# Kernel optimization log

Hardware: AMD Instinct MI355X
Metric: run time of the kernel (lower is better)

## Reference

```python
import jax, jax.numpy as jnp
import numpy as np

D_MODEL = 1024
NHEAD = 16
HEAD_DIM = D_MODEL // NHEAD


def setup_inputs() -> dict:
    key = jax.random.key(0)
    ks = jax.random.split(key, 9)
    B, N = 2, 2048
    x = jax.random.normal(ks[0], (B, N, D_MODEL), dtype=jnp.float32)
    s = 1.0 / np.sqrt(D_MODEL)
    Wq = jax.random.normal(ks[1], (D_MODEL, D_MODEL), dtype=jnp.float32) * s
    bq = jnp.zeros((D_MODEL,), dtype=jnp.float32)
    Wk = jax.random.normal(ks[2], (D_MODEL, D_MODEL), dtype=jnp.float32) * s
    bk = jnp.zeros((D_MODEL,), dtype=jnp.float32)
    Wv = jax.random.normal(ks[3], (D_MODEL, D_MODEL), dtype=jnp.float32) * s
    bv = jnp.zeros((D_MODEL,), dtype=jnp.float32)
    Wo = jax.random.normal(ks[4], (D_MODEL, D_MODEL), dtype=jnp.float32) * s
    bo = jnp.zeros((D_MODEL,), dtype=jnp.float32)
    return {"x": x, "Wq": Wq, "bq": bq, "Wk": Wk, "bk": bk,
            "Wv": Wv, "bv": bv, "Wo": Wo, "bo": bo}


def reference(x, Wq, bq, Wk, bk, Wv, bv, Wo, bo):
    B, N, C = x.shape
    H, Dh = NHEAD, HEAD_DIM
    scale = 1.0 / np.sqrt(Dh)

    def split_heads(t):
        # [B, N, C] -> [B, H, N, Dh]
        return t.reshape(B, N, H, Dh).transpose(0, 2, 1, 3)

    q = split_heads(x @ Wq.T + bq)
    k = split_heads(x @ Wk.T + bk)
    v = split_heads(x @ Wv.T + bv)

    # bipolar transform on Q/K before scores
    qb = (q - 0.5) * 2.0
    kb = (k - 0.5) * 2.0

    scores = jnp.einsum('bhqd,bhkd->bhqk', qb, kb) * scale  # [B,H,N,N]
    attn = jax.nn.softmax(scores, axis=-1)
    out = jnp.einsum('bhqk,bhkd->bhqd', attn, v)  # [B,H,N,Dh]
    out = out.transpose(0, 2, 1, 3).reshape(B, N, C)
    return out @ Wo.T + bo
```

## Files before the change

kernel.cpp:

```cpp
#include <hip/hip_runtime.h>
#include <cstdint>
#include <math.h>

typedef __attribute__((ext_vector_type(8))) short short8;
typedef __attribute__((ext_vector_type(4))) short shortx4;
typedef __attribute__((ext_vector_type(4))) float floatx4;
typedef __attribute__((ext_vector_type(16))) float floatx16;

#define D_MODEL 1024
#define NHEAD   16
#define HDIM    64
#define BATCH   2
#define SEQ     2048
#define MTOT    (BATCH*SEQ)

#if __has_builtin(__builtin_amdgcn_exp2f)
#define EXP2(x) __builtin_amdgcn_exp2f(x)
#else
#define EXP2(x) exp2f(x)
#endif

__device__ __forceinline__ short f2bf(float f) {
    union { float f; uint32_t u; } v; v.f = f;
    uint32_t u = v.u;
    uint32_t r = (u + 0x7fffu + ((u >> 16) & 1u)) >> 16;
    return (short)(uint16_t)r;
}

__device__ __forceinline__ unsigned pk2(float lo, float hi) {
    union { float f; uint32_t u; } x, y; x.f = lo; y.f = hi;
    return __builtin_amdgcn_perm(y.u + 0x8000u, x.u + 0x8000u, 0x07060302u);
}

__device__ __forceinline__ void async16(const short* g, short* l) {
    __builtin_amdgcn_global_load_lds((__attribute__((address_space(1))) void*)g,
                                     (__attribute__((address_space(3))) void*)l,
                                     16, 0, 0);
}

__global__ __launch_bounds__(256) void cast_all_kernel(
    const float* __restrict__ x,  const float* __restrict__ Wq, const float* __restrict__ Wk,
    const float* __restrict__ Wv, const float* __restrict__ Wo,
    short* __restrict__ xb, short* __restrict__ wqb, short* __restrict__ wkb,
    short* __restrict__ wvb, short* __restrict__ wob)
{
    const int i = blockIdx.x * 256 + threadIdx.x;
    const float* src; short* dst; int off;
    if (i < 524288) { src = x; dst = xb; off = i; }
    else {
        const int j = i - 524288;
        const int seg = j >> 17, o = j & 131071;
        src = (seg == 0) ? Wq : (seg == 1) ? Wk : (seg == 2) ? Wv : Wo;
        dst = (seg == 0) ? wqb : (seg == 1) ? wkb : (seg == 2) ? wvb : wob;
        off = o;
    }
    const floatx4* p = (const floatx4*)(src + (size_t)off * 8);
    floatx4 a = p[0], b = p[1];
    short8 r;
    r[0]=f2bf(a[0]); r[1]=f2bf(a[1]); r[2]=f2bf(a[2]); r[3]=f2bf(a[3]);
    r[4]=f2bf(b[0]); r[5]=f2bf(b[1]); r[6]=f2bf(b[2]); r[7]=f2bf(b[3]);
    *(short8*)(dst + (size_t)off * 8) = r;
}

__global__ __launch_bounds__(256, 3) void qkv_gemm_kernel(
    const short* __restrict__ Xb,
    const short* __restrict__ Wqb, const short* __restrict__ Wkb, const short* __restrict__ Wvb,
    const float* __restrict__ bq, const float* __restrict__ bk, const float* __restrict__ bv,
    short* __restrict__ Qo, short* __restrict__ Ko, short* __restrict__ Vo)
{
    const int mode = blockIdx.z;
    const short* W    = (mode == 0) ? Wqb : (mode == 1) ? Wkb : Wvb;
    const float* bias = (mode == 0) ? bq  : (mode == 1) ? bk  : bv;

    const int m_t = blockIdx.y * 128;
    const int n_t = blockIdx.x * 128;
    const int tid = threadIdx.x;
    const int lane = tid & 63, laneM = lane & 15, quad = lane >> 4;
    const int wave = tid >> 6;
    const int wm = (wave >> 1) * 64, wn = (wave & 1) * 64;

    __shared__ short la[2][128][4][8];
    __shared__ short lb[2][128][4][8];

    floatx4 acc[4][4];
#pragma unroll
    for (int mb = 0; mb < 4; mb++)
#pragma unroll
        for (int nb = 0; nb < 4; nb++) acc[mb][nb] = (floatx4){0.f,0.f,0.f,0.f};

#define QSTAGE(bf, kk)                                                                  \
    {                                                                                   \
        int c = tid;                                                                    \
        async16(Xb + (size_t)(m_t + (c >> 2)) * D_MODEL + (kk) + ((((c & 3) ^ ((c >> 3) & 3))) * 8), \
                &la[bf][0][0][0] + c * 8);                                              \
        c = tid + 256;                                                                  \
        async16(Xb + (size_t)(m_t + (c >> 2)) * D_MODEL + (kk) + ((((c & 3) ^ ((c >> 3) & 3))) * 8), \
                &la[bf][0][0][0] + c * 8);                                              \
        c = tid;                                                                        \
        async16(W  + (size_t)(n_t + (c >> 2)) * D_MODEL + (kk) + ((((c & 3) ^ ((c >> 3) & 3))) * 8), \
                &lb[bf][0][0][0] + c * 8);                                              \
        c = tid + 256;                                                                  \
        async16(W  + (size_t)(n_t + (c >> 2)) * D_MODEL + (kk) + ((((c & 3) ^ ((c >> 3) & 3))) * 8), \
                &lb[bf][0][0][0] + c * 8);                                              \
    }

    QSTAGE(0, 0)

    const int swz = (laneM >> 1) & 3;
    for (int it = 0; it < 32; ++it) {
        const int bf = it & 1;
        __syncthreads();

        short8 af[4], bfv[4];
#pragma unroll
        for (int mb = 0; mb < 4; mb++) af[mb]  = *(const short8*)&la[bf][wm + mb*16 + laneM][quad ^ swz][0];
#pragma unroll
        for (int nb = 0; nb < 4; nb++) bfv[nb] = *(const short8*)&lb[bf][wn + nb*16 + laneM][quad ^ swz][0];

        if (it < 31) QSTAGE(bf ^ 1, (it + 1) * 32)

#pragma unroll
        for (int mb = 0; mb < 4; mb++)
#pragma unroll
            for (int nb = 0; nb < 4; nb++)
                acc[mb][nb] = __builtin_amdgcn_mfma_f32_16x16x32_bf16(af[mb], bfv[nb], acc[mb][nb], 0, 0, 0);
    }
#undef QSTAGE

    if (mode == 2) {
#pragma unroll
        for (int nb = 0; nb < 4; nb++) {
            const int col = n_t + wn + nb*16 + laneM;
            const float bb = bias[col];
            const int h = col >> 6, d = col & 63;
#pragma unroll
            for (int mb = 0; mb < 4; mb++) {
                const int row0 = m_t + wm + mb*16 + quad*4;
                const int bi = row0 >> 11, seq0 = row0 & 2047;
                shortx4 sv;
#pragma unroll
                for (int r = 0; r < 4; r++) sv[r] = f2bf(acc[mb][nb][r] + bb);
                *(shortx4*)(Vo + ((size_t)(bi*NHEAD + h) * HDIM + d) * SEQ + seq0) = sv;
            }
        }
    } else {
        short* out = (mode == 0) ? Qo : Ko;
#pragma unroll
        for (int nb = 0; nb < 4; nb++) {
            const int col = n_t + wn + nb*16 + laneM;
            const float bb = bias[col];
            const int h = col >> 6, d = col & 63;
#pragma unroll
            for (int mb = 0; mb < 4; mb++) {
                const int row0 = m_t + wm + mb*16 + quad*4;
#pragma unroll
                for (int r = 0; r < 4; r++) {
                    float v = acc[mb][nb][r] + bb;
                    v = (mode == 0) ? (2.0f*v - 1.0f) * 0.18033688011112042f
                                    : (2.0f*v - 1.0f);
                    const int m = row0 + r;
                    const int bi = m >> 11, seq = m & 2047;
                    out[((size_t)(bi*NHEAD + h) * SEQ + seq) * HDIM + d] = f2bf(v);
                }
            }
        }
    }
}

__global__ __launch_bounds__(256, 3) void out_gemm_kernel(
    const short* __restrict__ Ab, const short* __restrict__ Wb,
    const float* __restrict__ bias, float* __restrict__ out)
{
    const int m_t = blockIdx.y * 128;
    const int n_t = blockIdx.x * 64;
    const int tid = threadIdx.x;
    const int lane = tid & 63, laneM = lane & 15, quad = lane >> 4;
    const int wave = tid >> 6;
    const int wm = (wave >> 1) * 64, wn = (wave & 1) * 32;

    __shared__ short la[2][128][4][8];
    __shared__ short lb[2][64][4][8];

    floatx4 acc[4][2];
#pragma unroll
    for (int mb = 0; mb < 4; mb++)
#pragma unroll
        for (int nb = 0; nb < 2; nb++) acc[mb][nb] = (floatx4){0.f,0.f,0.f,0.f};

#define OSTAGE(bf, kk)                                                                  \
    {                                                                                   \
        int c = tid;                                                                    \
        async16(Ab + (size_t)(m_t + (c >> 2)) * D_MODEL + (kk) + ((((c & 3) ^ ((c >> 3) & 3))) * 8), \
                &la[bf][0][0][0] + c * 8);                                              \
        c = tid + 256;                                                                  \
        async16(Ab + (size_t)(m_t + (c >> 2)) * D_MODEL + (kk) + ((((c & 3) ^ ((c >> 3) & 3))) * 8), \
                &la[bf][0][0][0] + c * 8);                                              \
        c = tid;                                                                        \
        async16(Wb + (size_t)(n_t + (c >> 2)) * D_MODEL + (kk) + ((((c & 3) ^ ((c >> 3) & 3))) * 8), \
                &lb[bf][0][0][0] + c * 8);                                              \
    }

    OSTAGE(0, 0)

    const int swz = (laneM >> 1) & 3;
    for (int it = 0; it < 32; ++it) {
        const int bf = it & 1;
        __syncthreads();

        short8 af[4], bfv[2];
#pragma unroll
        for (int mb = 0; mb < 4; mb++) af[mb]  = *(const short8*)&la[bf][wm + mb*16 + laneM][quad ^ swz][0];
#pragma unroll
        for (int nb = 0; nb < 2; nb++) bfv[nb] = *(const short8*)&lb[bf][wn + nb*16 + laneM][quad ^ swz][0];

        if (it < 31) OSTAGE(bf ^ 1, (it + 1) * 32)

#pragma unroll
        for (int mb = 0; mb < 4; mb++)
#pragma unroll
            for (int nb = 0; nb < 2; nb++)
                acc[mb][nb] = __builtin_amdgcn_mfma_f32_16x16x32_bf16(af[mb], bfv[nb], acc[mb][nb], 0, 0, 0);
    }
#undef OSTAGE

#pragma unroll
    for (int nb = 0; nb < 2; nb++) {
        const int col = n_t + wn + nb*16 + laneM;
        const float bb = bias[col];
#pragma unroll
        for (int mb = 0; mb < 4; mb++) {
            const int row0 = m_t + wm + mb*16 + quad*4;
#pragma unroll
            for (int r = 0; r < 4; r++)
                out[(size_t)(row0 + r) * D_MODEL + col] = acc[mb][nb][r] + bb;
        }
    }
}

__global__ __launch_bounds__(512, 4) void attn_kernel(const short* __restrict__ Qb,
                                                      const short* __restrict__ Kb,
                                                      const short* __restrict__ Vt,
                                                      short* __restrict__ Ob)
{
    const int bh = blockIdx.y;
    const int q0 = blockIdx.x * 128;
    const int tid = threadIdx.x;
    const int wave = tid >> 6, lane = tid & 63;
    const int l31 = lane & 31;
    const bool hi = (lane >> 5) != 0;
    const int qg = wave & 3, par = wave >> 2;

    __shared__ short kt[2][2][8][64][8];
    __shared__ short vtl[2][2][8][64][8];

    const short* Kbase = Kb + (size_t)bh * SEQ * HDIM;
    const short* Vbase = Vt + (size_t)bh * HDIM * SEQ;

    const short* Qp = Qb + ((size_t)bh * SEQ + q0 + qg*32 + l31) * HDIM + (hi ? 8 : 0);
    short8 qf[4];
#pragma unroll
    for (int ks = 0; ks < 4; ks++) qf[ks] = *(const short8*)(Qp + ks*16);

    floatx16 o0, o1;
#pragma unroll
    for (int r = 0; r < 16; r++) { o0[r] = 0.f; o1[r] = 0.f; }
    float rsum = 0.f;

#define STAGE(slot, kk)                                                                   \
    {                                                                                     \
        const int c = tid;                                                                \
        async16(Kbase + (size_t)((kk) + (c & 63)) * HDIM + (c >> 6) * 8,                  \
                &kt[0][slot][0][0][0] + c * 8);                                           \
        async16(Kbase + (size_t)((kk) + 64 + (c & 63)) * HDIM + (c >> 6) * 8,             \
                &kt[1][slot][0][0][0] + c * 8);                                           \
        async16(Vbase + (size_t)(c & 63) * SEQ + (kk) + (c >> 6) * 8,                     \
                &vtl[0][slot][0][0][0] + c * 8);                                          \
        async16(Vbase + (size_t)(c & 63) * SEQ + (kk) + 64 + (c >> 6) * 8,                \
                &vtl[1][slot][0][0][0] + c * 8);                                          \
    }

    STAGE(0, 0)

    for (int i = 0; i < 16; ++i) {
        const int slot = i & 1;
        __syncthreads();
        if (i < 15) STAGE(slot ^ 1, (i + 1) * 128)

        floatx16 s0, s1;
#pragma unroll
        for (int r = 0; r < 16; r++) { s0[r] = 0.f; s1[r] = 0.f; }
#pragma unroll
        for (int ks = 0; ks < 4; ks++) {
            const short8 a0 = *(const short8*)&kt[par][slot][2*ks + hi][l31][0];
            const short8 a1 = *(const short8*)&kt[par][slot][2*ks + hi][32 + l31][0];
            s0 = __builtin_amdgcn_mfma_f32_32x32x16_bf16(a0, qf[ks], s0, 0, 0, 0);
            s1 = __builtin_amdgcn_mfma_f32_32x32x16_bf16(a1, qf[ks], s1, 0, 0, 0);
        }

        unsigned p[16];
#pragma unroll
        for (int i2 = 0; i2 < 8; i2++) {
            const float a0 = EXP2(s0[2*i2]), b0 = EXP2(s0[2*i2+1]);
            const float a1 = EXP2(s1[2*i2]), b1 = EXP2(s1[2*i2+1]);
            rsum += (a0 + b0) + (a1 + b1);
            p[i2]     = pk2(a0, b0);
            p[8 + i2] = pk2(a1, b1);
        }

        unsigned fu[4][4];
#pragma unroll
        for (int g = 0; g < 4; g++) {
            const int base = (g >> 1) * 8 + (g & 1) * 4;
#pragma unroll
            for (int j = 0; j < 2; j++) {
                const unsigned pa = p[base + j], pb = p[base + j + 2];
                const unsigned pre = hi ? pa : pb;
                const unsigned sw = (unsigned)__shfl_xor((int)pre, 32, 64);
                fu[g][j]     = hi ? sw : pa;
                fu[g][j + 2] = hi ? pb : sw;
            }
        }

#pragma unroll
        for (int ks = 0; ks < 4; ks++) {
            union { unsigned u[4]; short8 s; } pf;
            pf.u[0] = fu[ks][0]; pf.u[1] = fu[ks][1]; pf.u[2] = fu[ks][2]; pf.u[3] = fu[ks][3];
            const short8 v0 = *(const short8*)&vtl[par][slot][2*ks + hi][l31][0];
            const short8 v1 = *(const short8*)&vtl[par][slot][2*ks + hi][32 + l31][0];
            o0 = __builtin_amdgcn_mfma_f32_32x32x16_bf16(pf.s, v0, o0, 0, 0, 0);
            o1 = __builtin_amdgcn_mfma_f32_32x32x16_bf16(pf.s, v1, o1, 0, 0, 0);
        }
    }
#undef STAGE

    rsum += __shfl_xor(rsum, 32, 64);

    float* mO = (float*)&kt[0][0][0][0][0];
    float* rS = (float*)&vtl[0][0][0][0][0];
    __syncthreads();
    if (par == 1) {
#pragma unroll
        for (int r = 0; r < 16; r++) {
            const int qr = (r & 3) + 8 * (r >> 2) + (hi ? 4 : 0);
            mO[(qg*32 + qr)*64 + l31]      = o0[r];
            mO[(qg*32 + qr)*64 + 32 + l31] = o1[r];
        }
        if (!hi) rS[qg*32 + l31] = rsum;
    }
    __syncthreads();
    if (par == 0) {
        const float inv = 1.0f / (rsum + rS[qg*32 + l31]);
        const int b = bh >> 4, h = bh & 15;
#pragma unroll
        for (int r = 0; r < 16; r++) {
            const int qr = (r & 3) + 8 * (r >> 2) + (hi ? 4 : 0);
            const float invr = __shfl(inv, qr, 64);
            const float v0 = o0[r] + mO[(qg*32 + qr)*64 + l31];
            const float v1 = o1[r] + mO[(qg*32 + qr)*64 + 32 + l31];
            const int seq = q0 + qg*32 + qr;
            short* dst = Ob + ((size_t)(b * SEQ + seq)) * D_MODEL + h * HDIM + l31;
            dst[0]  = f2bf(v0 * invr);
            dst[32] = f2bf(v1 * invr);
        }
    }
}

extern "C" void kernel_launch(void* const* d_in, const int* in_sizes, int n_in,
                              void* d_out, int out_size, void* d_ws, size_t ws_size,
                              hipStream_t stream)
{
    const float* x  = (const float*)d_in[0];
    const float* Wq = (const float*)d_in[1];
    const float* bq = (const float*)d_in[2];
    const float* Wk = (const float*)d_in[3];
    const float* bk = (const float*)d_in[4];
    const float* Wv = (const float*)d_in[5];
    const float* bv = (const float*)d_in[6];
    const float* Wo = (const float*)d_in[7];
    const float* bo = (const float*)d_in[8];
    float* out = (float*)d_out;

    short* ws = (short*)d_ws;
    const size_t NX = (size_t)MTOT * D_MODEL;
    const size_t NW = (size_t)D_MODEL * D_MODEL;
    short* xb  = ws;
    short* wqb = xb  + NX;
    short* wkb = wqb + NW;
    short* wvb = wkb + NW;
    short* wob = wvb + NW;
    short* Qb  = wob + NW;
    short* Kb  = Qb  + NX;
    short* Vt  = Kb  + NX;
    short* Ob  = Vt  + NX;

    cast_all_kernel<<<dim3(4096), 256, 0, stream>>>(x, Wq, Wk, Wv, Wo, xb, wqb, wkb, wvb, wob);
    qkv_gemm_kernel<<<dim3(8, 32, 3), 256, 0, stream>>>(xb, wqb, wkb, wvb, bq, bk, bv, Qb, Kb, Vt);
    attn_kernel<<<dim3(16, 32), 512, 0, stream>>>(Qb, Kb, Vt, Ob);
    out_gemm_kernel<<<dim3(16, 32), 256, 0, stream>>>(Ob, wob, bo, out);
}
```

Before: 191.7 us.

## Split attention key range across four wave groups with 1024-thread blocks

The attention block grows from 512 to 1024 threads, so four wave groups each handle a quarter of every 256-key chunk instead of two groups handling halves of 128-key chunks. The double-buffered async prefetch is dropped for a single-buffer load, sync, compute, sync loop, and the partial outputs and row sums are combined through a multi-step shared-memory reduction. The aim is more parallelism per query tile and fewer loop iterations. The cost is that load latency is no longer overlapped with compute, plus extra barriers in the reduction and higher register and occupancy pressure at 1024 threads.

```diff
diff --git a/kernel.cpp b/kernel.cpp
--- a/kernel.cpp
+++ b/kernel.cpp
@@ -237,10 +237,10 @@
     }
 }
 
-__global__ __launch_bounds__(512, 4) void attn_kernel(const short* __restrict__ Qb,
-                                                      const short* __restrict__ Kb,
-                                                      const short* __restrict__ Vt,
-                                                      short* __restrict__ Ob)
+__global__ __launch_bounds__(1024, 8) void attn_kernel(const short* __restrict__ Qb,
+                                                       const short* __restrict__ Kb,
+                                                       const short* __restrict__ Vt,
+                                                       short* __restrict__ Ob)
 {
     const int bh = blockIdx.y;
     const int q0 = blockIdx.x * 128;
@@ -250,8 +250,11 @@
     const bool hi = (lane >> 5) != 0;
     const int qg = wave & 3, par = wave >> 2;
 
-    __shared__ short kt[2][2][8][64][8];
-    __shared__ short vtl[2][2][8][64][8];
+    __shared__ union {
+        struct { short kt[4][8][64][8]; short vtl[4][8][64][8]; } s;
+        float mO[2][4][32][64];
+        float rsAll[3][128];
+    } u;
 
     const short* Kbase = Kb + (size_t)bh * SEQ * HDIM;
     const short* Vbase = Vt + (size_t)bh * HDIM * SEQ;
@@ -266,33 +269,31 @@
     for (int r = 0; r < 16; r++) { o0[r] = 0.f; o1[r] = 0.f; }
     float rsum = 0.f;
 
-#define STAGE(slot, kk)                                                                   \
-    {                                                                                     \
-        const int c = tid;                                                                \
-        async16(Kbase + (size_t)((kk) + (c & 63)) * HDIM + (c >> 6) * 8,                  \
-                &kt[0][slot][0][0][0] + c * 8);                                           \
-        async16(Kbase + (size_t)((kk) + 64 + (c & 63)) * HDIM + (c >> 6) * 8,             \
-                &kt[1][slot][0][0][0] + c * 8);                                           \
-        async16(Vbase + (size_t)(c & 63) * SEQ + (kk) + (c >> 6) * 8,                     \
-                &vtl[0][slot][0][0][0] + c * 8);                                          \
-        async16(Vbase + (size_t)(c & 63) * SEQ + (kk) + 64 + (c >> 6) * 8,                \
-                &vtl[1][slot][0][0][0] + c * 8);                                          \
-    }
-
-    STAGE(0, 0)
-
-    for (int i = 0; i < 16; ++i) {
-        const int slot = i & 1;
+#define STAGE(kk)                                                                          \
+    {                                                                                      \
+        int c = tid;                                                                       \
+        async16(Kbase + (size_t)((kk) + ((c >> 9) << 6) + (c & 63)) * HDIM + (((c >> 6) & 7) * 8), \
+                &u.s.kt[0][0][0][0] + c * 8);                                              \
+        async16(Vbase + (size_t)(c & 63) * SEQ + (kk) + ((c >> 9) << 6) + (((c >> 6) & 7) * 8), \
+                &u.s.vtl[0][0][0][0] + c * 8);                                             \
+        c = tid + 1024;                                                                    \
+        async16(Kbase + (size_t)((kk) + ((c >> 9) << 6) + (c & 63)) * HDIM + (((c >> 6) & 7) * 8), \
+                &u.s.kt[0][0][0][0] + c * 8);                                              \
+        async16(Vbase + (size_t)(c & 63) * SEQ + (kk) + ((c >> 9) << 6) + (((c >> 6) & 7) * 8), \
+                &u.s.vtl[0][0][0][0] + c * 8);                                             \
+    }
+
+    for (int i = 0; i < 8; ++i) {
+        STAGE(i * 256)
         __syncthreads();
-        if (i < 15) STAGE(slot ^ 1, (i + 1) * 128)
 
         floatx16 s0, s1;
 #pragma unroll
         for (int r = 0; r < 16; r++) { s0[r] = 0.f; s1[r] = 0.f; }
 #pragma unroll
         for (int ks = 0; ks < 4; ks++) {
-            const short8 a0 = *(const short8*)&kt[par][slot][2*ks + hi][l31][0];
-            const short8 a1 = *(const short8*)&kt[par][slot][2*ks + hi][32 + l31][0];
+            const short8 a0 = *(const short8*)&u.s.kt[par][2*ks + hi][l31][0];
+            const short8 a1 = *(const short8*)&u.s.kt[par][2*ks + hi][32 + l31][0];
             s0 = __builtin_amdgcn_mfma_f32_32x32x16_bf16(a0, qf[ks], s0, 0, 0, 0);
             s1 = __builtin_amdgcn_mfma_f32_32x32x16_bf16(a1, qf[ks], s1, 0, 0, 0);
         }
@@ -323,40 +324,63 @@
 
 #pragma unroll
         for (int ks = 0; ks < 4; ks++) {
-            union { unsigned u[4]; short8 s; } pf;
-            pf.u[0] = fu[ks][0]; pf.u[1] = fu[ks][1]; pf.u[2] = fu[ks][2]; pf.u[3] = fu[ks][3];
-            const short8 v0 = *(const short8*)&vtl[par][slot][2*ks + hi][l31][0];
-            const short8 v1 = *(const short8*)&vtl[par][slot][2*ks + hi][32 + l31][0];
-            o0 = __builtin_amdgcn_mfma_f32_32x32x16_bf16(pf.s, v0, o0, 0, 0, 0);
-            o1 = __builtin_amdgcn_mfma_f32_32x32x16_bf16(pf.s, v1, o1, 0, 0, 0);
-        }
+            union { unsigned u4[4]; short8 s8; } pf;
+            pf.u4[0] = fu[ks][0]; pf.u4[1] = fu[ks][1]; pf.u4[2] = fu[ks][2]; pf.u4[3] = fu[ks][3];
+            const short8 v0 = *(const short8*)&u.s.vtl[par][2*ks + hi][l31][0];
+            const short8 v1 = *(const short8*)&u.s.vtl[par][2*ks + hi][32 + l31][0];
+            o0 = __builtin_amdgcn_mfma_f32_32x32x16_bf16(pf.s8, v0, o0, 0, 0, 0);
+            o1 = __builtin_amdgcn_mfma_f32_32x32x16_bf16(pf.s8, v1, o1, 0, 0, 0);
+        }
+
+        __syncthreads();
     }
 #undef STAGE
 
     rsum += __shfl_xor(rsum, 32, 64);
 
-    float* mO = (float*)&kt[0][0][0][0][0];
-    float* rS = (float*)&vtl[0][0][0][0][0];
+    if (par >= 1 && !hi) u.rsAll[par - 1][qg*32 + l31] = rsum;
+    __syncthreads();
+    if (par == 0)
+        rsum += u.rsAll[0][qg*32 + l31] + u.rsAll[1][qg*32 + l31] + u.rsAll[2][qg*32 + l31];
+    __syncthreads();
+
+    if (par >= 2) {
+        const int sel = par - 2;
+#pragma unroll
+        for (int r = 0; r < 16; r++) {
+            const int qr = (r & 3) + 8 * (r >> 2) + (hi ? 4 : 0);
+            u.mO[sel][qg][qr][l31]      = o0[r];
+            u.mO[sel][qg][qr][32 + l31] = o1[r];
+        }
+    }
+    __syncthreads();
+    if (par < 2) {
+#pragma unroll
+        for (int r = 0; r < 16; r++) {
+            const int qr = (r & 3) + 8 * (r >> 2) + (hi ? 4 : 0);
+            o0[r] += u.mO[par][qg][qr][l31];
+            o1[r] += u.mO[par][qg][qr][32 + l31];
+        }
+    }
     __syncthreads();
     if (par == 1) {
 #pragma unroll
         for (int r = 0; r < 16; r++) {
             const int qr = (r & 3) + 8 * (r >> 2) + (hi ? 4 : 0);
-            mO[(qg*32 + qr)*64 + l31]      = o0[r];
-            mO[(qg*32 + qr)*64 + 32 + l31] = o1[r];
-        }
-        if (!hi) rS[qg*32 + l31] = rsum;
+            u.mO[0][qg][qr][l31]      = o0[r];
+            u.mO[0][qg][qr][32 + l31] = o1[r];
+        }
     }
     __syncthreads();
     if (par == 0) {
-        const float inv = 1.0f / (rsum + rS[qg*32 + l31]);
+        const float inv = 1.0f / rsum;
         const int b = bh >> 4, h = bh & 15;
 #pragma unroll
         for (int r = 0; r < 16; r++) {
             const int qr = (r & 3) + 8 * (r >> 2) + (hi ? 4 : 0);
             const float invr = __shfl(inv, qr, 64);
-            const float v0 = o0[r] + mO[(qg*32 + qr)*64 + l31];
-            const float v1 = o1[r] + mO[(qg*32 + qr)*64 + 32 + l31];
+            const float v0 = o0[r] + u.mO[0][qg][qr][l31];
+            const float v1 = o1[r] + u.mO[0][qg][qr][32 + l31];
             const int seq = q0 + qg*32 + qr;
             short* dst = Ob + ((size_t)(b * SEQ + seq)) * D_MODEL + h * HDIM + l31;
             dst[0]  = f2bf(v0 * invr);
@@ -395,6 +419,6 @@
 
     cast_all_kernel<<<dim3(4096), 256, 0, stream>>>(x, Wq, Wk, Wv, Wo, xb, wqb, wkb, wvb, wob);
     qkv_gemm_kernel<<<dim3(8, 32, 3), 256, 0, stream>>>(xb, wqb, wkb, wvb, bq, bk, bv, Qb, Kb, Vt);
-    attn_kernel<<<dim3(16, 32), 512, 0, stream>>>(Qb, Kb, Vt, Ob);
+    attn_kernel<<<dim3(16, 32), 1024, 0, stream>>>(Qb, Kb, Vt, Ob);
     out_gemm_kernel<<<dim3(16, 32), 256, 0, stream>>>(Ob, wob, bo, out);
 }
```

New measurement: 469.0 us. 2.45x slower.
